# Kernel tuning notes

Hardware: AMD Instinct MI355X
Metric: run time of the kernel (lower is better)

## Reference

```python
import jax, jax.numpy as jnp
import numpy as np

B, S, D, H, DFF = 2, 2048, 512, 8, 2048
DK = D // H
EPS = 1e-6  # LayerNormalization eps


def _ln(x, a, b):
    # torch: alpha * (x - mean) / (std + eps) + bias, std is unbiased (ddof=1)
    m = jnp.mean(x, axis=-1, keepdims=True)
    s = jnp.std(x, axis=-1, keepdims=True, ddof=1)
    return a * (x - m) / (s + EPS) + b


def _mha(Q, K, V, mask, Wq, bq, Wk, bk, Wv, bv, Wo, bo):
    Bq, Sq = Q.shape[0], Q.shape[1]
    Sk = K.shape[1]
    q = (Q @ Wq + bq).reshape(Bq, Sq, H, DK).transpose(0, 2, 1, 3)  # bhqd
    k = (K @ Wk + bk).reshape(Bq, Sk, H, DK).transpose(0, 2, 1, 3)  # bhkd
    v = (V @ Wv + bv).reshape(Bq, Sk, H, DK).transpose(0, 2, 1, 3)  # bhkd
    scores = jnp.einsum('bhqd,bhkd->bhqk', q, k) / jnp.sqrt(jnp.float32(DK))
    scores = jnp.where(mask == 0, -jnp.inf, scores)  # masked_fill(mask==0, -inf)
    attn = jax.nn.softmax(scores, axis=-1)  # dropout is identity in eval
    out = jnp.einsum('bhqk,bhkd->bhqd', attn, v)
    out = out.transpose(0, 2, 1, 3).reshape(Bq, Sq, D)
    return out @ Wo + bo


def setup_inputs() -> dict:
    key = jax.random.key(0)
    ks = jax.random.split(key, 20)
    sc = 0.02
    inp = {
        'x': jax.random.normal(ks[0], (B, S, D), jnp.float32),
        'encoder_output': jax.random.normal(ks[1], (B, S, D), jnp.float32),
        'encoder_output_mask': jnp.broadcast_to(jnp.ones((S, S), jnp.int32), (B, 1, S, S)),
        'decoder_mask': jnp.broadcast_to(jnp.tril(jnp.ones((S, S), jnp.int32)), (B, 1, S, S)),
        'sa_Wq': jax.random.normal(ks[2], (D, D), jnp.float32) * sc,
        'sa_bq': jnp.zeros((D,), jnp.float32),
        'sa_Wk': jax.random.normal(ks[3], (D, D), jnp.float32) * sc,
        'sa_bk': jnp.zeros((D,), jnp.float32),
        'sa_Wv': jax.random.normal(ks[4], (D, D), jnp.float32) * sc,
        'sa_bv': jnp.zeros((D,), jnp.float32),
        'sa_Wo': jax.random.normal(ks[5], (D, D), jnp.float32) * sc,
        'sa_bo': jnp.zeros((D,), jnp.float32),
        'ca_Wq': jax.random.normal(ks[6], (D, D), jnp.float32) * sc,
        'ca_bq': jnp.zeros((D,), jnp.float32),
        'ca_Wk': jax.random.normal(ks[7], (D, D), jnp.float32) * sc,
        'ca_bk': jnp.zeros((D,), jnp.float32),
        'ca_Wv': jax.random.normal(ks[8], (D, D), jnp.float32) * sc,
        'ca_bv': jnp.zeros((D,), jnp.float32),
        'ca_Wo': jax.random.normal(ks[9], (D, D), jnp.float32) * sc,
        'ca_bo': jnp.zeros((D,), jnp.float32),
        'ff_W1': jax.random.normal(ks[10], (D, DFF), jnp.float32) * sc,
        'ff_b1': jnp.zeros((DFF,), jnp.float32),
        'ff_W2': jax.random.normal(ks[11], (DFF, D), jnp.float32) * sc,
        'ff_b2': jnp.zeros((D,), jnp.float32),
        'ln0_a': jnp.ones((1,), jnp.float32), 'ln0_b': jnp.zeros((1,), jnp.float32),
        'ln1_a': jnp.ones((1,), jnp.float32), 'ln1_b': jnp.zeros((1,), jnp.float32),
        'ln2_a': jnp.ones((1,), jnp.float32), 'ln2_b': jnp.zeros((1,), jnp.float32),
    }
    return inp


def reference(x, encoder_output, encoder_output_mask, decoder_mask,
              sa_Wq, sa_bq, sa_Wk, sa_bk, sa_Wv, sa_bv, sa_Wo, sa_bo,
              ca_Wq, ca_bq, ca_Wk, ca_bk, ca_Wv, ca_bv, ca_Wo, ca_bo,
              ff_W1, ff_b1, ff_W2, ff_b2,
              ln0_a, ln0_b, ln1_a, ln1_b, ln2_a, ln2_b):
    # Residual 0: pre-norm self-attention (dropout = identity in eval)
    n = _ln(x, ln0_a, ln0_b)
    x = x + _mha(n, n, n, decoder_mask, sa_Wq, sa_bq, sa_Wk, sa_bk, sa_Wv, sa_bv, sa_Wo, sa_bo)
    # Residual 1: pre-norm cross-attention
    n = _ln(x, ln1_a, ln1_b)
    x = x + _mha(n, encoder_output, encoder_output, encoder_output_mask,
                 ca_Wq, ca_bq, ca_Wk, ca_bk, ca_Wv, ca_bv, ca_Wo, ca_bo)
    # Residual 2: pre-norm FFN (Linear -> ReLU -> Linear)
    n = _ln(x, ln2_a, ln2_b)
    x = x + (jax.nn.relu(n @ ff_W1 + ff_b1) @ ff_W2 + ff_b2)
    return x
```

## Files before the change

### kernel.cpp

```cpp
#include <hip/hip_runtime.h>
#include <hip/hip_bf16.h>

typedef __bf16 bf16_t;
typedef __bf16 bf16x8_t __attribute__((ext_vector_type(8)));
typedef float f32x4_t __attribute__((ext_vector_type(4)));

static constexpr int B_ = 2, S_ = 2048, D_ = 512, H_ = 8, DK_ = 64, DFF_ = 2048;
static constexpr int M_ = B_ * S_;
static constexpr float QSCALE = 0.125f * 1.44269504f;

__device__ __forceinline__ unsigned pkbf(float a, float b) {
  union { bf16_t h; unsigned short u; } x, y;
  x.h = (bf16_t)a; y.h = (bf16_t)b;
  return (unsigned)x.u | ((unsigned)y.u << 16);
}

__device__ __forceinline__ void async16(bf16_t* lds, const bf16_t* g) {
  __builtin_amdgcn_global_load_lds((__attribute__((address_space(1))) void*)g,
                                   (__attribute__((address_space(3))) void*)lds,
                                   16, 0, 0);
}

__global__ __launch_bounds__(256) void ln_kernel(const float* __restrict__ x,
                                                 const float* __restrict__ ga,
                                                 const float* __restrict__ gb,
                                                 bf16_t* __restrict__ out) {
  const int row = blockIdx.x * 4 + (threadIdx.x >> 6);
  const int lane = threadIdx.x & 63;
  const float4* xr = (const float4*)(x + (long)row * D_);
  float4 v0 = xr[lane * 2];
  float4 v1 = xr[lane * 2 + 1];
  float s = v0.x + v0.y + v0.z + v0.w + v1.x + v1.y + v1.z + v1.w;
  float ss = v0.x * v0.x + v0.y * v0.y + v0.z * v0.z + v0.w * v0.w +
             v1.x * v1.x + v1.y * v1.y + v1.z * v1.z + v1.w * v1.w;
#pragma unroll
  for (int m = 1; m < 64; m <<= 1) {
    s += __shfl_xor(s, m);
    ss += __shfl_xor(ss, m);
  }
  const float mean = s * (1.0f / 512.0f);
  float var = (ss - 512.0f * mean * mean) * (1.0f / 511.0f);
  var = fmaxf(var, 0.0f);
  const float sc = ga[0] / (sqrtf(var) + 1e-6f);
  const float sh = gb[0] - mean * sc;
  alignas(16) bf16_t y[8];
  y[0] = (bf16_t)(v0.x * sc + sh);
  y[1] = (bf16_t)(v0.y * sc + sh);
  y[2] = (bf16_t)(v0.z * sc + sh);
  y[3] = (bf16_t)(v0.w * sc + sh);
  y[4] = (bf16_t)(v1.x * sc + sh);
  y[5] = (bf16_t)(v1.y * sc + sh);
  y[6] = (bf16_t)(v1.z * sc + sh);
  y[7] = (bf16_t)(v1.w * sc + sh);
  ((uint4*)(out + (long)row * D_))[lane] = *(uint4*)y;
}

__global__ __launch_bounds__(256) void cvt_bf16(const float* __restrict__ x,
                                                bf16_t* __restrict__ y) {
  const long i = ((long)blockIdx.x * 256 + threadIdx.x) * 8;
  float4 a = *(const float4*)(x + i);
  float4 b = *(const float4*)(x + i + 4);
  alignas(16) bf16_t t[8];
  t[0] = (bf16_t)a.x; t[1] = (bf16_t)a.y; t[2] = (bf16_t)a.z; t[3] = (bf16_t)a.w;
  t[4] = (bf16_t)b.x; t[5] = (bf16_t)b.y; t[6] = (bf16_t)b.z; t[7] = (bf16_t)b.w;
  *(uint4*)(y + i) = *(uint4*)t;
}

__device__ __forceinline__ void wtrans_body(const float* __restrict__ W,
                                            bf16_t* __restrict__ Wt, int K, int N,
                                            int k0, int n0) {
  constexpr int LDT = 65;
  __shared__ float T[64 * LDT];
  const int tid = threadIdx.x;
#pragma unroll
  for (int p = 0; p < 4; ++p) {
    int e = p * 1024 + tid * 4;
    int kr = e >> 6, nc = e & 63;
    float4 f = *(const float4*)(W + (long)(k0 + kr) * N + n0 + nc);
    T[kr * LDT + nc + 0] = f.x;
    T[kr * LDT + nc + 1] = f.y;
    T[kr * LDT + nc + 2] = f.z;
    T[kr * LDT + nc + 3] = f.w;
  }
  __syncthreads();
#pragma unroll
  for (int p = 0; p < 4; ++p) {
    int e = p * 1024 + tid * 4;
    int nr = e >> 6, kc = e & 63;
    alignas(8) bf16_t t[4];
#pragma unroll
    for (int j = 0; j < 4; ++j) t[j] = (bf16_t)T[(kc + j) * LDT + nr];
    *(uint2*)(Wt + (long)(n0 + nr) * K + k0 + kc) = *(uint2*)t;
  }
}

struct WPA { const float* W[10]; bf16_t* T[10]; };
__global__ __launch_bounds__(256) void wprep(WPA a) {
  const int x = blockIdx.x;
  if (x < 512) {
    const int wi = x >> 6, t = x & 63;
    wtrans_body(a.W[wi], a.T[wi], 512, 512, (t >> 3) * 64, (t & 7) * 64);
  } else if (x < 768) {
    const int t = x - 512;
    wtrans_body(a.W[8], a.T[8], 512, 2048, (t & 7) * 64, (t >> 3) * 64);
  } else {
    const int t = x - 768;
    wtrans_body(a.W[9], a.T[9], 2048, 512, (t & 31) * 64, (t >> 5) * 64);
  }
}

__global__ __launch_bounds__(256) void vtrans(const bf16_t* __restrict__ v,
                                              bf16_t* __restrict__ vt) {
  constexpr int LDT = 66;
  __shared__ bf16_t T[64 * LDT];
  const int tid = threadIdx.x;
  const int bh = blockIdx.y, b = bh >> 3, h = bh & 7;
  const int s0 = blockIdx.x * 64;
#pragma unroll
  for (int p = 0; p < 2; ++p) {
    int e = p * 2048 + tid * 8;
    int sr = e >> 6, c = e & 63;
    uint4 u = *(const uint4*)(v + (long)(b * S_ + s0 + sr) * D_ + h * DK_ + c);
    bf16_t* pv = (bf16_t*)&u;
#pragma unroll
    for (int j = 0; j < 8; ++j) T[(c + j) * LDT + sr] = pv[j];
  }
  __syncthreads();
#pragma unroll
  for (int p = 0; p < 2; ++p) {
    int e = p * 2048 + tid * 8;
    int d = e >> 6, sc = e & 63;
    alignas(16) bf16_t t[8];
#pragma unroll
    for (int j = 0; j < 8; ++j) t[j] = T[d * LDT + sc + j];
    *(uint4*)(vt + ((long)bh * DK_ + d) * S_ + s0 + sc) = *(uint4*)t;
  }
}

struct GArg {
  const bf16_t* A;
  const bf16_t* Wt;
  const float* bias;
  const float* res;
  void* out;
  float oscale;
};

template <int MODE>
__global__ __launch_bounds__(256, 4) void gemm_bt(GArg g0, GArg g1, GArg g2,
                                                  int M, int N, int K) {
  __shared__ bf16_t As[2][64 * 64];
  __shared__ bf16_t Bs[2][64 * 64];
  GArg g = (blockIdx.z == 0) ? g0 : (blockIdx.z == 1) ? g1 : g2;
  const int tid = threadIdx.x;
  const int wave = tid >> 6, lane = tid & 63, quad = lane >> 4, l15 = lane & 15;
  const long m0 = (long)blockIdx.x * 64;
  const long n0 = (long)blockIdx.y * 64;
  const int wm = (wave >> 1) * 32;
  const int wn = (wave & 1) * 32;

  const int r8 = lane >> 3;
  const int cg = (lane & 7) ^ r8;
  const bf16_t* Ab = g.A + m0 * (long)K + cg * 8;
  const bf16_t* Bb = g.Wt + n0 * (long)K + cg * 8;

  auto stage = [&](int buf, int k0) {
#pragma unroll
    for (int c = 0; c < 2; ++c) {
      const int row = wave * 16 + c * 8;
      async16(&As[buf][row * 64], Ab + (long)(row + r8) * K + k0);
      async16(&Bs[buf][row * 64], Bb + (long)(row + r8) * K + k0);
    }
  };

  f32x4_t acc[2][2];
#pragma unroll
  for (int i = 0; i < 2; ++i)
#pragma unroll
    for (int j = 0; j < 2; ++j) acc[i][j] = (f32x4_t){0.f, 0.f, 0.f, 0.f};

  const int KT = K >> 6;
  stage(0, 0);
  for (int kt = 0; kt < KT; ++kt) {
    __syncthreads();
    if (kt + 1 < KT) stage((kt + 1) & 1, (kt + 1) * 64);
    const bf16_t* Al = &As[kt & 1][0];
    const bf16_t* Bl = &Bs[kt & 1][0];
    bf16x8_t af[2][2], bfr[2][2];
#pragma unroll
    for (int ks = 0; ks < 2; ++ks) {
      const int sc = ((ks * 4 + quad) ^ (l15 & 7)) * 8;
#pragma unroll
      for (int i = 0; i < 2; ++i) {
        af[ks][i] = *(const bf16x8_t*)&Al[(wm + i * 16 + l15) * 64 + sc];
        bfr[ks][i] = *(const bf16x8_t*)&Bl[(wn + i * 16 + l15) * 64 + sc];
      }
    }
#pragma unroll
    for (int ks = 0; ks < 2; ++ks)
#pragma unroll
      for (int i = 0; i < 2; ++i)
#pragma unroll
        for (int j = 0; j < 2; ++j)
          acc[i][j] = __builtin_amdgcn_mfma_f32_16x16x32_bf16(af[ks][i], bfr[ks][j], acc[i][j], 0, 0, 0);
  }

#pragma unroll
  for (int i = 0; i < 2; ++i) {
#pragma unroll
    for (int j = 0; j < 2; ++j) {
      const long col = n0 + wn + j * 16 + l15;
      const float bv = g.bias[col];
#pragma unroll
      for (int r = 0; r < 4; ++r) {
        const long row = m0 + wm + i * 16 + quad * 4 + r;
        float v = acc[i][j][r] + bv;
        if constexpr (MODE == 1) v = fmaxf(v, 0.f);
        if constexpr (MODE == 2) {
          ((float*)g.out)[row * N + col] = v + g.res[row * N + col];
        } else {
          ((bf16_t*)g.out)[row * N + col] = (bf16_t)(v * g.oscale);
        }
      }
    }
  }
}

template <bool CAUSAL>
__global__ __launch_bounds__(256, 4) void flash_attn(const bf16_t* __restrict__ Q,
                                                     const bf16_t* __restrict__ Kg,
                                                     const bf16_t* __restrict__ Vt,
                                                     float* __restrict__ po,
                                                     float* __restrict__ pl) {
  __shared__ bf16_t Ks[2][64 * 64];
  __shared__ bf16_t Vs[2][64 * 64];
  __shared__ bf16_t Ps[4][16 * 64];
  const int tid = threadIdx.x, wave = tid >> 6, lane = tid & 63;
  const int quad = lane >> 4, l15 = lane & 15;
  const int bh = blockIdx.y, b = bh >> 3, h = bh & 7;
  const int qt = CAUSAL ? (31 - (int)blockIdx.x) : (int)blockIdx.x;
  const int chunk = blockIdx.z;
  const int ntt = CAUSAL ? (qt + 1) : 32;
  const int n0t = (ntt + 1) >> 1;
  const int tstart = chunk ? n0t : 0;
  const int tend = chunk ? ntt : n0t;
  const long pbase = ((long)chunk * 16 + bh) * 32 + qt;

  if (tstart >= tend) {
#pragma unroll
    for (int i = 0; i < 4; ++i)
      *(f32x4_t*)&po[pbase * 4096 + tid * 16 + i * 4] = (f32x4_t){0.f, 0.f, 0.f, 0.f};
    if (tid < 64) pl[pbase * 64 + tid] = 0.f;
    return;
  }

  const int q0 = qt * 64;
  const int qw = q0 + wave * 16;
  const long base = (long)b * S_ * D_ + (long)h * DK_;
  const long vtbase = (long)bh * DK_ * S_;

  const bf16_t* Qp = Q + base + (long)(qw + l15) * D_ + quad * 8;
  const bf16x8_t qf0 = *(const bf16x8_t*)(Qp);
  const bf16x8_t qf1 = *(const bf16x8_t*)(Qp + 32);

  const int r8 = lane >> 3;
  const int cg8 = (lane & 7) ^ r8;
  const bf16_t* Kb = Kg + base + cg8 * 8;
  const bf16_t* Vb = Vt + vtbase + cg8 * 8;

  auto stage = [&](int buf, int t) {
    const int kk0 = t * 64;
#pragma unroll
    for (int c = 0; c < 2; ++c) {
      const int row = wave * 16 + c * 8;
      async16(&Ks[buf][row * 64], Kb + (long)(kk0 + row + r8) * D_);
      async16(&Vs[buf][row * 64], Vb + (long)(row + r8) * S_ + kk0);
    }
  };

  float li = 0.f;
  f32x4_t o[4];
#pragma unroll
  for (int db = 0; db < 4; ++db) o[db] = (f32x4_t){0.f, 0.f, 0.f, 0.f};

  bf16_t* Pw = &Ps[wave][0];
  const int pws = l15 * 64 + (quad & 1) * 4;
  const int pq7 = l15 & 7;

  stage(0, tstart);
  for (int t = tstart; t < tend; ++t) {
    const int buf = (t - tstart) & 1;
    __syncthreads();
    if (t + 1 < tend) stage(buf ^ 1, t + 1);
    const bf16_t* Kt = &Ks[buf][0];
    const bf16_t* Vl = &Vs[buf][0];
    const int kk0 = t * 64;

    f32x4_t st[4];
#pragma unroll
    for (int nb = 0; nb < 4; ++nb) {
      f32x4_t a = (f32x4_t){0.f, 0.f, 0.f, 0.f};
#pragma unroll
      for (int ks = 0; ks < 2; ++ks) {
        const int scf = ((ks * 4 + quad) ^ (l15 & 7)) * 8;
        const bf16x8_t kf = *(const bf16x8_t*)&Kt[(nb * 16 + l15) * 64 + scf];
        a = __builtin_amdgcn_mfma_f32_16x16x32_bf16(kf, ks ? qf1 : qf0, a, 0, 0, 0);
      }
      st[nb] = a;
    }

    const bool domask = CAUSAL && (t == qt);
#pragma unroll
    for (int nb = 0; nb < 4; ++nb)
#pragma unroll
      for (int r = 0; r < 4; ++r) {
        float v = st[nb][r];
        if (domask && (kk0 + nb * 16 + quad * 4 + r > qw + l15)) v = -1e30f;
        const float p = exp2f(v);
        st[nb][r] = p;
        li += p;
      }

#pragma unroll
    for (int nb = 0; nb < 4; ++nb) {
      uint2 w;
      w.x = pkbf(st[nb][0], st[nb][1]);
      w.y = pkbf(st[nb][2], st[nb][3]);
      const int ck = nb * 2 + (quad >> 1);
      *(uint2*)&Pw[pws + (ck ^ pq7) * 8 - (quad & 1) * 4 + (quad & 1) * 4] = w;
    }
    const bf16x8_t pf0 = *(const bf16x8_t*)&Pw[l15 * 64 + ((quad) ^ pq7) * 8];
    const bf16x8_t pf1 = *(const bf16x8_t*)&Pw[l15 * 64 + ((4 + quad) ^ pq7) * 8];
#pragma unroll
    for (int ks = 0; ks < 2; ++ks) {
      const bf16x8_t pf = ks ? pf1 : pf0;
#pragma unroll
      for (int db = 0; db < 4; ++db) {
        const int scf = ((ks * 4 + quad) ^ (l15 & 7)) * 8;
        const bf16x8_t vf = *(const bf16x8_t*)&Vl[(db * 16 + l15) * 64 + scf];
        o[db] = __builtin_amdgcn_mfma_f32_16x16x32_bf16(vf, pf, o[db], 0, 0, 0);
      }
    }
  }

  li += __shfl_xor(li, 16);
  li += __shfl_xor(li, 32);

#pragma unroll
  for (int db = 0; db < 4; ++db)
    *(f32x4_t*)&po[pbase * 4096 + (wave * 16 + l15) * 64 + db * 16 + quad * 4] = o[db];
  if (quad == 0) pl[pbase * 64 + wave * 16 + l15] = li;
}

__global__ __launch_bounds__(256) void merge_attn(const float* __restrict__ po,
                                                  const float* __restrict__ pl,
                                                  bf16_t* __restrict__ O) {
  const int qt = blockIdx.x, bh = blockIdx.y, b = bh >> 3, h = bh & 7;
  const long p0 = ((long)bh) * 32 + qt;
  const long p1 = ((long)16 + bh) * 32 + qt;
  const int t = threadIdx.x;
  const int q = t >> 2, d0 = (t & 3) * 16;
  const float inv = 1.0f / (pl[p0 * 64 + q] + pl[p1 * 64 + q]);
  const long i0 = p0 * 4096 + q * 64 + d0;
  const long i1 = p1 * 4096 + q * 64 + d0;
  alignas(16) bf16_t out[16];
#pragma unroll
  for (int j = 0; j < 4; ++j) {
    f32x4_t a = *(const f32x4_t*)&po[i0 + j * 4];
    f32x4_t c = *(const f32x4_t*)&po[i1 + j * 4];
#pragma unroll
    for (int r = 0; r < 4; ++r) out[j * 4 + r] = (bf16_t)((a[r] + c[r]) * inv);
  }
  const long row = (long)b * S_ + qt * 64 + q;
  *(uint4*)(O + row * D_ + h * DK_ + d0) = *(uint4*)&out[0];
  *(uint4*)(O + row * D_ + h * DK_ + d0 + 8) = *(uint4*)&out[8];
}

extern "C" void kernel_launch(void* const* d_in, const int* in_sizes, int n_in,
                              void* d_out, int out_size, void* d_ws, size_t ws_size,
                              hipStream_t stream) {
  const float* x    = (const float*)d_in[0];
  const float* enc  = (const float*)d_in[1];
  const float* saWq = (const float*)d_in[4];  const float* sabq = (const float*)d_in[5];
  const float* saWk = (const float*)d_in[6];  const float* sabk = (const float*)d_in[7];
  const float* saWv = (const float*)d_in[8];  const float* sabv = (const float*)d_in[9];
  const float* saWo = (const float*)d_in[10]; const float* sabo = (const float*)d_in[11];
  const float* caWq = (const float*)d_in[12]; const float* cabq = (const float*)d_in[13];
  const float* caWk = (const float*)d_in[14]; const float* cabk = (const float*)d_in[15];
  const float* caWv = (const float*)d_in[16]; const float* cabv = (const float*)d_in[17];
  const float* caWo = (const float*)d_in[18]; const float* cabo = (const float*)d_in[19];
  const float* ffW1 = (const float*)d_in[20]; const float* ffb1 = (const float*)d_in[21];
  const float* ffW2 = (const float*)d_in[22]; const float* ffb2 = (const float*)d_in[23];
  const float* ln0a = (const float*)d_in[24]; const float* ln0b = (const float*)d_in[25];
  const float* ln1a = (const float*)d_in[26]; const float* ln1b = (const float*)d_in[27];
  const float* ln2a = (const float*)d_in[28]; const float* ln2b = (const float*)d_in[29];

  char* ws = (char*)d_ws;
  size_t off = 0;
  auto alloc = [&](size_t bytes) -> void* {
    void* p = ws + off;
    off += (bytes + 255) & ~(size_t)255;
    return p;
  };
  bf16_t* wt_saq = (bf16_t*)alloc(512 * 512 * 2);
  bf16_t* wt_sak = (bf16_t*)alloc(512 * 512 * 2);
  bf16_t* wt_sav = (bf16_t*)alloc(512 * 512 * 2);
  bf16_t* wt_sao = (bf16_t*)alloc(512 * 512 * 2);
  bf16_t* wt_caq = (bf16_t*)alloc(512 * 512 * 2);
  bf16_t* wt_cak = (bf16_t*)alloc(512 * 512 * 2);
  bf16_t* wt_cav = (bf16_t*)alloc(512 * 512 * 2);
  bf16_t* wt_cao = (bf16_t*)alloc(512 * 512 * 2);
  bf16_t* wt_f1  = (bf16_t*)alloc((size_t)512 * 2048 * 2);
  bf16_t* wt_f2  = (bf16_t*)alloc((size_t)2048 * 512 * 2);
  bf16_t* enc_b  = (bf16_t*)alloc((size_t)M_ * D_ * 2);
  bf16_t* nbuf   = (bf16_t*)alloc((size_t)M_ * D_ * 2);
  bf16_t* qb     = (bf16_t*)alloc((size_t)M_ * D_ * 2);
  bf16_t* kb     = (bf16_t*)alloc((size_t)M_ * D_ * 2);
  bf16_t* vb     = (bf16_t*)alloc((size_t)M_ * D_ * 2);
  bf16_t* vtb    = (bf16_t*)alloc((size_t)M_ * D_ * 2);
  bf16_t* attnb  = (bf16_t*)alloc((size_t)M_ * D_ * 2);
  bf16_t* hid    = (bf16_t*)alloc((size_t)M_ * DFF_ * 2);
  float*  x1     = (float*)alloc((size_t)M_ * D_ * 4);
  float*  x2     = (float*)alloc((size_t)M_ * D_ * 4);
  float*  pl     = (float*)alloc(2 * 16 * 32 * 64 * 4);
  float*  po     = (float*)hid;

  {
    WPA a;
    a.W[0] = saWq; a.T[0] = wt_saq;
    a.W[1] = saWk; a.T[1] = wt_sak;
    a.W[2] = saWv; a.T[2] = wt_sav;
    a.W[3] = saWo; a.T[3] = wt_sao;
    a.W[4] = caWq; a.T[4] = wt_caq;
    a.W[5] = caWk; a.T[5] = wt_cak;
    a.W[6] = caWv; a.T[6] = wt_cav;
    a.W[7] = caWo; a.T[7] = wt_cao;
    a.W[8] = ffW1; a.T[8] = wt_f1;
    a.W[9] = ffW2; a.T[9] = wt_f2;
    wprep<<<1024, 256, 0, stream>>>(a);
  }
  cvt_bf16<<<1024, 256, 0, stream>>>(enc, enc_b);

  ln_kernel<<<1024, 256, 0, stream>>>(x, ln0a, ln0b, nbuf);
  {
    GArg z0{nbuf, wt_saq, sabq, nullptr, qb, QSCALE};
    GArg z1{nbuf, wt_sak, sabk, nullptr, kb, 1.0f};
    GArg z2{nbuf, wt_sav, sabv, nullptr, vb, 1.0f};
    gemm_bt<0><<<dim3(64, 8, 3), 256, 0, stream>>>(z0, z1, z2, M_, 512, 512);
  }
  vtrans<<<dim3(32, 16), 256, 0, stream>>>(vb, vtb);
  flash_attn<true><<<dim3(32, 16, 2), 256, 0, stream>>>(qb, kb, vtb, po, pl);
  merge_attn<<<dim3(32, 16), 256, 0, stream>>>(po, pl, attnb);
  {
    GArg o1{attnb, wt_sao, sabo, x, x1, 1.0f};
    gemm_bt<2><<<dim3(64, 8, 1), 256, 0, stream>>>(o1, o1, o1, M_, 512, 512);
  }

  ln_kernel<<<1024, 256, 0, stream>>>(x1, ln1a, ln1b, nbuf);
  {
    GArg c0{nbuf,  wt_caq, cabq, nullptr, qb, QSCALE};
    GArg c1{enc_b, wt_cak, cabk, nullptr, kb, 1.0f};
    GArg c2{enc_b, wt_cav, cabv, nullptr, vb, 1.0f};
    gemm_bt<0><<<dim3(64, 8, 3), 256, 0, stream>>>(c0, c1, c2, M_, 512, 512);
  }
  vtrans<<<dim3(32, 16), 256, 0, stream>>>(vb, vtb);
  flash_attn<false><<<dim3(32, 16, 2), 256, 0, stream>>>(qb, kb, vtb, po, pl);
  merge_attn<<<dim3(32, 16), 256, 0, stream>>>(po, pl, attnb);
  {
    GArg o2{attnb, wt_cao, cabo, x1, x2, 1.0f};
    gemm_bt<2><<<dim3(64, 8, 1), 256, 0, stream>>>(o2, o2, o2, M_, 512, 512);
  }

  ln_kernel<<<1024, 256, 0, stream>>>(x2, ln2a, ln2b, nbuf);
  {
    GArg f1{nbuf, wt_f1, ffb1, nullptr, hid, 1.0f};
    gemm_bt<1><<<dim3(64, 32, 1), 256, 0, stream>>>(f1, f1, f1, M_, DFF_, 512);
  }
  {
    GArg f2{hid, wt_f2, ffb2, x2, d_out, 1.0f};
    gemm_bt<2><<<dim3(64, 8, 1), 256, 0, stream>>>(f2, f2, f2, M_, 512, DFF_);
  }
}
```

Measured before the change: 364.4 us.

## Enlarge GEMM and attention tiles with triple-buffered vmcnt-gated async loads

GEMM tiles widen from 64x64 to 64x128 per block, and flash attention handles 128 query rows per block (32 per wave), so each staged K/V tile is reused across more queries. Both kernels move from double to triple buffering, with an explicit s_waitcnt vmcnt plus s_barrier in place of __syncthreads, so loads can run two stages ahead. The causal split and the partial-output layout are reworked to per-row indexing, which also drops the empty-chunk early exit. The cost is more LDS and more registers per block, with launch bounds lowered to 2 blocks per SM, and fewer blocks in the grid.

Result: slower. 385.9 us (+5.9%).

```diff
diff --git a/kernel.cpp b/kernel.cpp
--- a/kernel.cpp
+++ b/kernel.cpp
@@ -8,6 +8,8 @@
 static constexpr int B_ = 2, S_ = 2048, D_ = 512, H_ = 8, DK_ = 64, DFF_ = 2048;
 static constexpr int M_ = B_ * S_;
 static constexpr float QSCALE = 0.125f * 1.44269504f;
+
+#define VMCNT_BARRIER(N) asm volatile("s_waitcnt vmcnt(" #N ")\n\ts_barrier" ::: "memory")
 
 __device__ __forceinline__ unsigned pkbf(float a, float b) {
   union { bf16_t h; unsigned short u; } x, y;
@@ -147,17 +149,17 @@
 };
 
 template <int MODE>
-__global__ __launch_bounds__(256, 4) void gemm_bt(GArg g0, GArg g1, GArg g2,
+__global__ __launch_bounds__(256, 2) void gemm_bt(GArg g0, GArg g1, GArg g2,
                                                   int M, int N, int K) {
-  __shared__ bf16_t As[2][64 * 64];
-  __shared__ bf16_t Bs[2][64 * 64];
+  __shared__ bf16_t As[3][64 * 64];
+  __shared__ bf16_t Bs[3][128 * 64];
   GArg g = (blockIdx.z == 0) ? g0 : (blockIdx.z == 1) ? g1 : g2;
   const int tid = threadIdx.x;
   const int wave = tid >> 6, lane = tid & 63, quad = lane >> 4, l15 = lane & 15;
   const long m0 = (long)blockIdx.x * 64;
-  const long n0 = (long)blockIdx.y * 64;
+  const long n0 = (long)blockIdx.y * 128;
   const int wm = (wave >> 1) * 32;
-  const int wn = (wave & 1) * 32;
+  const int wn = (wave & 1) * 64;
 
   const int r8 = lane >> 3;
   const int cg = (lane & 7) ^ r8;
@@ -169,46 +171,55 @@
     for (int c = 0; c < 2; ++c) {
       const int row = wave * 16 + c * 8;
       async16(&As[buf][row * 64], Ab + (long)(row + r8) * K + k0);
+    }
+#pragma unroll
+    for (int c = 0; c < 4; ++c) {
+      const int row = wave * 32 + c * 8;
       async16(&Bs[buf][row * 64], Bb + (long)(row + r8) * K + k0);
     }
   };
 
-  f32x4_t acc[2][2];
+  f32x4_t acc[2][4];
 #pragma unroll
   for (int i = 0; i < 2; ++i)
 #pragma unroll
-    for (int j = 0; j < 2; ++j) acc[i][j] = (f32x4_t){0.f, 0.f, 0.f, 0.f};
+    for (int j = 0; j < 4; ++j) acc[i][j] = (f32x4_t){0.f, 0.f, 0.f, 0.f};
 
   const int KT = K >> 6;
   stage(0, 0);
+  stage(1, 64);
+  int bc = 0;
   for (int kt = 0; kt < KT; ++kt) {
-    __syncthreads();
-    if (kt + 1 < KT) stage((kt + 1) & 1, (kt + 1) * 64);
-    const bf16_t* Al = &As[kt & 1][0];
-    const bf16_t* Bl = &Bs[kt & 1][0];
-    bf16x8_t af[2][2], bfr[2][2];
+    if (kt + 1 < KT) { VMCNT_BARRIER(6); } else { VMCNT_BARRIER(0); }
+    int bs = bc + 2; if (bs >= 3) bs -= 3;
+    if (kt + 2 < KT) stage(bs, (kt + 2) * 64);
+    const bf16_t* Al = &As[bc][0];
+    const bf16_t* Bl = &Bs[bc][0];
+    bf16x8_t af[2][2], bfr[2][4];
 #pragma unroll
     for (int ks = 0; ks < 2; ++ks) {
       const int sc = ((ks * 4 + quad) ^ (l15 & 7)) * 8;
 #pragma unroll
-      for (int i = 0; i < 2; ++i) {
+      for (int i = 0; i < 2; ++i)
         af[ks][i] = *(const bf16x8_t*)&Al[(wm + i * 16 + l15) * 64 + sc];
-        bfr[ks][i] = *(const bf16x8_t*)&Bl[(wn + i * 16 + l15) * 64 + sc];
-      }
+#pragma unroll
+      for (int j = 0; j < 4; ++j)
+        bfr[ks][j] = *(const bf16x8_t*)&Bl[(wn + j * 16 + l15) * 64 + sc];
     }
 #pragma unroll
     for (int ks = 0; ks < 2; ++ks)
 #pragma unroll
       for (int i = 0; i < 2; ++i)
 #pragma unroll
-        for (int j = 0; j < 2; ++j)
+        for (int j = 0; j < 4; ++j)
           acc[i][j] = __builtin_amdgcn_mfma_f32_16x16x32_bf16(af[ks][i], bfr[ks][j], acc[i][j], 0, 0, 0);
+    bc = (bc + 1 == 3) ? 0 : bc + 1;
   }
 
 #pragma unroll
   for (int i = 0; i < 2; ++i) {
 #pragma unroll
-    for (int j = 0; j < 2; ++j) {
+    for (int j = 0; j < 4; ++j) {
       const long col = n0 + wn + j * 16 + l15;
       const float bv = g.bias[col];
 #pragma unroll
@@ -227,41 +238,36 @@
 }
 
 template <bool CAUSAL>
-__global__ __launch_bounds__(256, 4) void flash_attn(const bf16_t* __restrict__ Q,
+__global__ __launch_bounds__(256, 2) void flash_attn(const bf16_t* __restrict__ Q,
                                                      const bf16_t* __restrict__ Kg,
                                                      const bf16_t* __restrict__ Vt,
                                                      float* __restrict__ po,
                                                      float* __restrict__ pl) {
-  __shared__ bf16_t Ks[2][64 * 64];
-  __shared__ bf16_t Vs[2][64 * 64];
-  __shared__ bf16_t Ps[4][16 * 64];
+  __shared__ bf16_t Ks[3][64 * 64];
+  __shared__ bf16_t Vs[3][64 * 64];
+  __shared__ bf16_t Ps[4][32 * 64];
   const int tid = threadIdx.x, wave = tid >> 6, lane = tid & 63;
   const int quad = lane >> 4, l15 = lane & 15;
   const int bh = blockIdx.y, b = bh >> 3, h = bh & 7;
-  const int qt = CAUSAL ? (31 - (int)blockIdx.x) : (int)blockIdx.x;
+  const int qt = CAUSAL ? (15 - (int)blockIdx.x) : (int)blockIdx.x;
   const int chunk = blockIdx.z;
-  const int ntt = CAUSAL ? (qt + 1) : 32;
-  const int n0t = (ntt + 1) >> 1;
+  const int ntt = CAUSAL ? (2 * qt + 2) : 32;
+  const int n0t = ntt >> 1;
   const int tstart = chunk ? n0t : 0;
   const int tend = chunk ? ntt : n0t;
-  const long pbase = ((long)chunk * 16 + bh) * 32 + qt;
-
-  if (tstart >= tend) {
-#pragma unroll
-    for (int i = 0; i < 4; ++i)
-      *(f32x4_t*)&po[pbase * 4096 + tid * 16 + i * 4] = (f32x4_t){0.f, 0.f, 0.f, 0.f};
-    if (tid < 64) pl[pbase * 64 + tid] = 0.f;
-    return;
-  }
-
-  const int q0 = qt * 64;
-  const int qw = q0 + wave * 16;
+
+  const int q0 = qt * 128;
+  const int qw = q0 + wave * 32;
   const long base = (long)b * S_ * D_ + (long)h * DK_;
   const long vtbase = (long)bh * DK_ * S_;
-
-  const bf16_t* Qp = Q + base + (long)(qw + l15) * D_ + quad * 8;
-  const bf16x8_t qf0 = *(const bf16x8_t*)(Qp);
-  const bf16x8_t qf1 = *(const bf16x8_t*)(Qp + 32);
+  const long prow0 = ((long)(chunk * 16 + bh)) * 2048;
+
+  bf16x8_t qf[2][2];
+#pragma unroll
+  for (int qh = 0; qh < 2; ++qh)
+#pragma unroll
+    for (int ks = 0; ks < 2; ++ks)
+      qf[qh][ks] = *(const bf16x8_t*)(Q + base + (long)(qw + qh * 16 + l15) * D_ + ks * 32 + quad * 8);
 
   const int r8 = lane >> 3;
   const int cg8 = (lane & 7) ^ r8;
@@ -278,91 +284,106 @@
     }
   };
 
-  float li = 0.f;
-  f32x4_t o[4];
-#pragma unroll
-  for (int db = 0; db < 4; ++db) o[db] = (f32x4_t){0.f, 0.f, 0.f, 0.f};
+  float li[2] = {0.f, 0.f};
+  f32x4_t o[2][4];
+#pragma unroll
+  for (int qh = 0; qh < 2; ++qh)
+#pragma unroll
+    for (int db = 0; db < 4; ++db) o[qh][db] = (f32x4_t){0.f, 0.f, 0.f, 0.f};
 
   bf16_t* Pw = &Ps[wave][0];
-  const int pws = l15 * 64 + (quad & 1) * 4;
   const int pq7 = l15 & 7;
 
   stage(0, tstart);
+  if (tstart + 1 < tend) stage(1, tstart + 1);
+  int bc = 0;
   for (int t = tstart; t < tend; ++t) {
-    const int buf = (t - tstart) & 1;
-    __syncthreads();
-    if (t + 1 < tend) stage(buf ^ 1, t + 1);
-    const bf16_t* Kt = &Ks[buf][0];
-    const bf16_t* Vl = &Vs[buf][0];
+    if (t + 1 < tend) { VMCNT_BARRIER(4); } else { VMCNT_BARRIER(0); }
+    int bs = bc + 2; if (bs >= 3) bs -= 3;
+    if (t + 2 < tend) stage(bs, t + 2);
+    const bf16_t* Kt = &Ks[bc][0];
+    const bf16_t* Vl = &Vs[bc][0];
     const int kk0 = t * 64;
 
-    f32x4_t st[4];
-#pragma unroll
-    for (int nb = 0; nb < 4; ++nb) {
-      f32x4_t a = (f32x4_t){0.f, 0.f, 0.f, 0.f};
-#pragma unroll
-      for (int ks = 0; ks < 2; ++ks) {
-        const int scf = ((ks * 4 + quad) ^ (l15 & 7)) * 8;
-        const bf16x8_t kf = *(const bf16x8_t*)&Kt[(nb * 16 + l15) * 64 + scf];
-        a = __builtin_amdgcn_mfma_f32_16x16x32_bf16(kf, ks ? qf1 : qf0, a, 0, 0, 0);
+#pragma unroll
+    for (int qh = 0; qh < 2; ++qh) {
+      f32x4_t st[4];
+#pragma unroll
+      for (int nb = 0; nb < 4; ++nb) {
+        f32x4_t a = (f32x4_t){0.f, 0.f, 0.f, 0.f};
+#pragma unroll
+        for (int ks = 0; ks < 2; ++ks) {
+          const int scf = ((ks * 4 + quad) ^ (l15 & 7)) * 8;
+          const bf16x8_t kf = *(const bf16x8_t*)&Kt[(nb * 16 + l15) * 64 + scf];
+          a = __builtin_amdgcn_mfma_f32_16x16x32_bf16(kf, qf[qh][ks], a, 0, 0, 0);
+        }
+        st[nb] = a;
       }
-      st[nb] = a;
-    }
-
-    const bool domask = CAUSAL && (t == qt);
-#pragma unroll
-    for (int nb = 0; nb < 4; ++nb)
-#pragma unroll
-      for (int r = 0; r < 4; ++r) {
-        float v = st[nb][r];
-        if (domask && (kk0 + nb * 16 + quad * 4 + r > qw + l15)) v = -1e30f;
-        const float p = exp2f(v);
-        st[nb][r] = p;
-        li += p;
+      const bool domask = CAUSAL && (kk0 + 63 > qw + qh * 16);
+#pragma unroll
+      for (int nb = 0; nb < 4; ++nb)
+#pragma unroll
+        for (int r = 0; r < 4; ++r) {
+          float v = st[nb][r];
+          if (domask && (kk0 + nb * 16 + quad * 4 + r > qw + qh * 16 + l15)) v = -1e30f;
+          const float p = exp2f(v);
+          st[nb][r] = p;
+          li[qh] += p;
+        }
+      const int prow = (qh * 16 + l15) * 64;
+#pragma unroll
+      for (int nb = 0; nb < 4; ++nb) {
+        uint2 w;
+        w.x = pkbf(st[nb][0], st[nb][1]);
+        w.y = pkbf(st[nb][2], st[nb][3]);
+        const int ck = nb * 2 + (quad >> 1);
+        *(uint2*)&Pw[prow + (ck ^ pq7) * 8 + (quad & 1) * 4] = w;
       }
-
-#pragma unroll
-    for (int nb = 0; nb < 4; ++nb) {
-      uint2 w;
-      w.x = pkbf(st[nb][0], st[nb][1]);
-      w.y = pkbf(st[nb][2], st[nb][3]);
-      const int ck = nb * 2 + (quad >> 1);
-      *(uint2*)&Pw[pws + (ck ^ pq7) * 8 - (quad & 1) * 4 + (quad & 1) * 4] = w;
-    }
-    const bf16x8_t pf0 = *(const bf16x8_t*)&Pw[l15 * 64 + ((quad) ^ pq7) * 8];
-    const bf16x8_t pf1 = *(const bf16x8_t*)&Pw[l15 * 64 + ((4 + quad) ^ pq7) * 8];
+    }
+
+    bf16x8_t pf[2][2];
+#pragma unroll
+    for (int qh = 0; qh < 2; ++qh)
+#pragma unroll
+      for (int ks = 0; ks < 2; ++ks)
+        pf[qh][ks] = *(const bf16x8_t*)&Pw[(qh * 16 + l15) * 64 + (((ks * 4 + quad) ^ pq7)) * 8];
 #pragma unroll
     for (int ks = 0; ks < 2; ++ks) {
-      const bf16x8_t pf = ks ? pf1 : pf0;
 #pragma unroll
       for (int db = 0; db < 4; ++db) {
         const int scf = ((ks * 4 + quad) ^ (l15 & 7)) * 8;
         const bf16x8_t vf = *(const bf16x8_t*)&Vl[(db * 16 + l15) * 64 + scf];
-        o[db] = __builtin_amdgcn_mfma_f32_16x16x32_bf16(vf, pf, o[db], 0, 0, 0);
+#pragma unroll
+        for (int qh = 0; qh < 2; ++qh)
+          o[qh][db] = __builtin_amdgcn_mfma_f32_16x16x32_bf16(vf, pf[qh][ks], o[qh][db], 0, 0, 0);
       }
     }
-  }
-
-  li += __shfl_xor(li, 16);
-  li += __shfl_xor(li, 32);
-
-#pragma unroll
-  for (int db = 0; db < 4; ++db)
-    *(f32x4_t*)&po[pbase * 4096 + (wave * 16 + l15) * 64 + db * 16 + quad * 4] = o[db];
-  if (quad == 0) pl[pbase * 64 + wave * 16 + l15] = li;
+    bc = (bc + 1 == 3) ? 0 : bc + 1;
+  }
+
+#pragma unroll
+  for (int qh = 0; qh < 2; ++qh) {
+    li[qh] += __shfl_xor(li[qh], 16);
+    li[qh] += __shfl_xor(li[qh], 32);
+    const long pr = prow0 + qw + qh * 16 + l15;
+#pragma unroll
+    for (int db = 0; db < 4; ++db)
+      *(f32x4_t*)&po[pr * 64 + db * 16 + quad * 4] = o[qh][db];
+    if (quad == 0) pl[pr] = li[qh];
+  }
 }
 
 __global__ __launch_bounds__(256) void merge_attn(const float* __restrict__ po,
                                                   const float* __restrict__ pl,
                                                   bf16_t* __restrict__ O) {
   const int qt = blockIdx.x, bh = blockIdx.y, b = bh >> 3, h = bh & 7;
-  const long p0 = ((long)bh) * 32 + qt;
-  const long p1 = ((long)16 + bh) * 32 + qt;
   const int t = threadIdx.x;
-  const int q = t >> 2, d0 = (t & 3) * 16;
-  const float inv = 1.0f / (pl[p0 * 64 + q] + pl[p1 * 64 + q]);
-  const long i0 = p0 * 4096 + q * 64 + d0;
-  const long i1 = p1 * 4096 + q * 64 + d0;
+  const int q = qt * 64 + (t >> 2), d0 = (t & 3) * 16;
+  const long r0 = (long)bh * 2048 + q;
+  const long r1 = (long)(16 + bh) * 2048 + q;
+  const float inv = 1.0f / (pl[r0] + pl[r1]);
+  const long i0 = r0 * 64 + d0;
+  const long i1 = r1 * 64 + d0;
   alignas(16) bf16_t out[16];
 #pragma unroll
   for (int j = 0; j < 4; ++j) {
@@ -371,7 +392,7 @@
 #pragma unroll
     for (int r = 0; r < 4; ++r) out[j * 4 + r] = (bf16_t)((a[r] + c[r]) * inv);
   }
-  const long row = (long)b * S_ + qt * 64 + q;
+  const long row = (long)b * S_ + q;
   *(uint4*)(O + row * D_ + h * DK_ + d0) = *(uint4*)&out[0];
   *(uint4*)(O + row * D_ + h * DK_ + d0 + 8) = *(uint4*)&out[8];
 }
@@ -422,7 +443,7 @@
   bf16_t* hid    = (bf16_t*)alloc((size_t)M_ * DFF_ * 2);
   float*  x1     = (float*)alloc((size_t)M_ * D_ * 4);
   float*  x2     = (float*)alloc((size_t)M_ * D_ * 4);
-  float*  pl     = (float*)alloc(2 * 16 * 32 * 64 * 4);
+  float*  pl     = (float*)alloc(2 * 16 * 2048 * 4);
   float*  po     = (float*)hid;
 
   {
@@ -446,14 +467,14 @@
     GArg z0{nbuf, wt_saq, sabq, nullptr, qb, QSCALE};
     GArg z1{nbuf, wt_sak, sabk, nullptr, kb, 1.0f};
     GArg z2{nbuf, wt_sav, sabv, nullptr, vb, 1.0f};
-    gemm_bt<0><<<dim3(64, 8, 3), 256, 0, stream>>>(z0, z1, z2, M_, 512, 512);
+    gemm_bt<0><<<dim3(64, 4, 3), 256, 0, stream>>>(z0, z1, z2, M_, 512, 512);
   }
   vtrans<<<dim3(32, 16), 256, 0, stream>>>(vb, vtb);
-  flash_attn<true><<<dim3(32, 16, 2), 256, 0, stream>>>(qb, kb, vtb, po, pl);
+  flash_attn<true><<<dim3(16, 16, 2), 256, 0, stream>>>(qb, kb, vtb, po, pl);
   merge_attn<<<dim3(32, 16), 256, 0, stream>>>(po, pl, attnb);
   {
     GArg o1{attnb, wt_sao, sabo, x, x1, 1.0f};
-    gemm_bt<2><<<dim3(64, 8, 1), 256, 0, stream>>>(o1, o1, o1, M_, 512, 512);
+    gemm_bt<2><<<dim3(64, 4, 1), 256, 0, stream>>>(o1, o1, o1, M_, 512, 512);
   }
 
   ln_kernel<<<1024, 256, 0, stream>>>(x1, ln1a, ln1b, nbuf);
@@ -461,23 +482,23 @@
     GArg c0{nbuf,  wt_caq, cabq, nullptr, qb, QSCALE};
     GArg c1{enc_b, wt_cak, cabk, nullptr, kb, 1.0f};
     GArg c2{enc_b, wt_cav, cabv, nullptr, vb, 1.0f};
-    gemm_bt<0><<<dim3(64, 8, 3), 256, 0, stream>>>(c0, c1, c2, M_, 512, 512);
+    gemm_bt<0><<<dim3(64, 4, 3), 256, 0, stream>>>(c0, c1, c2, M_, 512, 512);
   }
   vtrans<<<dim3(32, 16), 256, 0, stream>>>(vb, vtb);
-  flash_attn<false><<<dim3(32, 16, 2), 256, 0, stream>>>(qb, kb, vtb, po, pl);
+  flash_attn<false><<<dim3(16, 16, 2), 256, 0, stream>>>(qb, kb, vtb, po, pl);
   merge_attn<<<dim3(32, 16), 256, 0, stream>>>(po, pl, attnb);
   {
     GArg o2{attnb, wt_cao, cabo, x1, x2, 1.0f};
-    gemm_bt<2><<<dim3(64, 8, 1), 256, 0, stream>>>(o2, o2, o2, M_, 512, 512);
+    gemm_bt<2><<<dim3(64, 4, 1), 256, 0, stream>>>(o2, o2, o2, M_, 512, 512);
   }
 
   ln_kernel<<<1024, 256, 0, stream>>>(x2, ln2a, ln2b, nbuf);
   {
     GArg f1{nbuf, wt_f1, ffb1, nullptr, hid, 1.0f};
-    gemm_bt<1><<<dim3(64, 32, 1), 256, 0, stream>>>(f1, f1, f1, M_, DFF_, 512);
+    gemm_bt<1><<<dim3(64, 16, 1), 256, 0, stream>>>(f1, f1, f1, M_, DFF_, 512);
   }
   {
     GArg f2{hid, wt_f2, ffb2, x2, d_out, 1.0f};
-    gemm_bt<2><<<dim3(64, 8, 1), 256, 0, stream>>>(f2, f2, f2, M_, 512, DFF_);
-  }
-}
+    gemm_bt<2><<<dim3(64, 4, 1), 256, 0, stream>>>(f2, f2, f2, M_, 512, DFF_);
+  }
+}
```
